# Kernel optimization log

Hardware: AMD Instinct MI355X
Metric: run time of the kernel (lower is better)

Reference implementation:

```python
import jax, jax.numpy as jnp
import numpy as np

DIM = 1024
HEADS = 16
DIM_HEAD = DIM // HEADS

def setup_inputs() -> dict:
    key = jax.random.key(0)
    k1, k2, k3 = jax.random.split(key, 3)
    x = jax.random.normal(k1, (2, 2048, DIM), dtype=jnp.float32)
    # nn.Linear(dim, 3*dim, bias=False): weight [3*dim, dim]; y = x @ W.T
    W_qkv = jax.random.normal(k2, (3 * DIM, DIM), dtype=jnp.float32) * (1.0 / np.sqrt(DIM))
    W_out = jax.random.normal(k3, (DIM, DIM), dtype=jnp.float32) * (1.0 / np.sqrt(DIM))
    return {"x": x, "W_qkv": W_qkv, "W_out": W_out}

def reference(x, W_qkv, W_out):
    b, s, _ = x.shape
    scale = DIM_HEAD ** -0.5
    qkv = x @ W_qkv.T                              # [b, s, 3*dim]
    q, k, v = jnp.split(qkv, 3, axis=-1)
    def to_heads(t):
        return t.reshape(b, s, HEADS, DIM_HEAD).transpose(0, 2, 1, 3)  # [b,h,s,d]
    q, k, v = map(to_heads, (q, k, v))
    scores = jnp.einsum('bhid,bhjd->bhij', q, k) * scale
    causal_mask = jnp.triu(jnp.ones((s, s), dtype=bool), k=1)
    scores = jnp.where(causal_mask, -jnp.inf, scores)
    attn = jax.nn.softmax(scores, axis=-1)
    out = jnp.einsum('bhij,bhjd->bhid', attn, v)
    out = out.transpose(0, 2, 1, 3).reshape(b, s, HEADS * DIM_HEAD)
    return out @ W_out.T
```

## Files before the change

kernel.cpp:

```cpp
#include <hip/hip_runtime.h>
#include <hip/hip_bf16.h>
#include <math.h>

using bf16 = __hip_bfloat16;
typedef __attribute__((ext_vector_type(8))) short bf16x8;
typedef __attribute__((ext_vector_type(4))) short bf16x4;
typedef __attribute__((ext_vector_type(4))) float f32x4;
typedef __attribute__((ext_vector_type(2))) int i32x2;

static __device__ __forceinline__ void gl_lds16(const void* g, void* l) {
  __builtin_amdgcn_global_load_lds(
      (const __attribute__((address_space(1))) unsigned int*)g,
      (__attribute__((address_space(3))) unsigned int*)l, 16, 0, 0);
}

#define MFMA16 __builtin_amdgcn_mfma_f32_16x16x32_bf16
#define MFMA16K16 __builtin_amdgcn_mfma_f32_16x16x16bf16_1k

static __device__ __forceinline__ short f2bf(float f) {
  return (short)((__builtin_bit_cast(unsigned int, f) + 0x8000u) >> 16);
}

__global__ __launch_bounds__(256) void cvt_all(
    const float* __restrict__ x, const float* __restrict__ wqkv,
    const float* __restrict__ wout, bf16* __restrict__ xb,
    bf16* __restrict__ wqkvb, bf16* __restrict__ woutb) {
  const int blk = blockIdx.x;
  const float* src;
  bf16* dst;
  int base;
  if (blk < 4096) {
    src = x; dst = xb; base = blk;
  } else if (blk < 7168) {
    src = wqkv; dst = wqkvb; base = blk - 4096;
  } else {
    src = wout; dst = woutb; base = blk - 7168;
  }
  const int i = (base * 256 + threadIdx.x) * 4;
  const float4 v = *(const float4*)(src + i);
  bf16x4 o;
  o.x = f2bf(v.x);
  o.y = f2bf(v.y);
  o.z = f2bf(v.z);
  o.w = f2bf(v.w);
  *(bf16x4*)(dst + i) = o;
}

template <int K>
static __device__ __forceinline__ void gemm_bt_acc(
    const bf16* __restrict__ A, const bf16* __restrict__ B,
    int rowA0, int rowB0, bf16* As, bf16* Bs, f32x4 acc[4][4]) {
  const int t = threadIdx.x;
  const int w = t >> 6, l = t & 63;
  const int quad = l >> 4, l16 = l & 15;
  const int wm = (w >> 1) * 64, wn = (w & 1) * 64;
  for (int k0 = 0; k0 < K; k0 += 64) {
    __syncthreads();
#pragma unroll
    for (int ii = 0; ii < 4; ii++) {
      const int c = t + ii * 256;
      const int row = c >> 3, pos = c & 7;
      const size_t off = (size_t)row * K + k0 + ((pos ^ (row & 7)) * 8);
      gl_lds16(A + (size_t)rowA0 * K + off, As + c * 8);
      gl_lds16(B + (size_t)rowB0 * K + off, Bs + c * 8);
    }
    __syncthreads();
#pragma unroll
    for (int kk2 = 0; kk2 < 2; kk2++) {
      bf16x8 af[4], bg[4];
#pragma unroll
      for (int i = 0; i < 4; i++) {
        const int rr = wm + i * 16 + l16;
        const int ci = (kk2 * 4 + quad) ^ (l16 & 7);
        af[i] = *(const bf16x8*)(As + rr * 64 + ci * 8);
      }
#pragma unroll
      for (int j = 0; j < 4; j++) {
        const int rr = wn + j * 16 + l16;
        const int ci = (kk2 * 4 + quad) ^ (l16 & 7);
        bg[j] = *(const bf16x8*)(Bs + rr * 64 + ci * 8);
      }
#pragma unroll
      for (int i = 0; i < 4; i++)
#pragma unroll
        for (int j = 0; j < 4; j++)
          acc[i][j] = MFMA16(af[i], bg[j], acc[i][j], 0, 0, 0);
    }
  }
}

__global__ __launch_bounds__(256, 3) void qkv_gemm(
    const bf16* __restrict__ x, const bf16* __restrict__ Wqkv,
    bf16* __restrict__ Qb, bf16* __restrict__ Kb, bf16* __restrict__ Vt) {
  __shared__ bf16 As[128 * 64];
  __shared__ bf16 Bs[128 * 64];
  f32x4 acc[4][4];
#pragma unroll
  for (int i = 0; i < 4; i++)
#pragma unroll
    for (int j = 0; j < 4; j++) acc[i][j] = (f32x4){0.f, 0.f, 0.f, 0.f};
  const int bm = blockIdx.x, bn = blockIdx.y;
  gemm_bt_acc<1024>(x, Wqkv, bm * 128, bn * 128, As, Bs, acc);

  const int t = threadIdx.x, w = t >> 6, l = t & 63;
  const int quad = l >> 4, l16 = l & 15;
  const int wm = (w >> 1) * 64, wn = (w & 1) * 64;
#pragma unroll
  for (int i = 0; i < 4; i++) {
    const int m0 = bm * 128 + wm + i * 16 + quad * 4;
    const int b = m0 >> 11, s0 = m0 & 2047;
#pragma unroll
    for (int j = 0; j < 4; j++) {
      const int n = bn * 128 + wn + j * 16 + l16;
      const int which = n >> 10;
      const int nn = n & 1023;
      const int h = nn >> 6, d = nn & 63;
      const int bh = b * 16 + h;
      if (which == 2) {
        bf16x4 v4;
#pragma unroll
        for (int r = 0; r < 4; r++)
          v4[r] = (short)__builtin_bit_cast(unsigned short,
                                            __float2bfloat16(acc[i][j][r]));
        *(bf16x4*)(Vt + ((size_t)bh * 64 + d) * 2048 + s0) = v4;
      } else {
        const float sc = (which == 0) ? 0.125f : 1.0f;
        bf16* dst = (which == 0) ? Qb : Kb;
#pragma unroll
        for (int r = 0; r < 4; r++)
          dst[((size_t)bh * 2048 + s0 + r) * 64 + d] =
              __float2bfloat16(acc[i][j][r] * sc);
      }
    }
  }
}

__global__ __launch_bounds__(256, 4) void attn_kernel(
    const bf16* __restrict__ Qb, const bf16* __restrict__ Kb,
    const bf16* __restrict__ Vt, bf16* __restrict__ attn) {
  __shared__ bf16 Ks[128 * 64];
  __shared__ bf16 Vts[64 * 128];
  const int x = blockIdx.x;
  const int bh = x & 31;
  const int T = x >> 5;
  const int s = T >> 3, r = T & 7;
  const int qt = s * 8 + ((s & 1) ? 7 - r : r);
  const int q0 = qt * 64;
  const int t = threadIdx.x, w = t >> 6, l = t & 63;
  const int quad = l >> 4, l16 = l & 15;
  const bf16x4 ones = {16256, 16256, 16256, 16256};
  const int b = bh >> 4, h = bh & 15;

  const int qrow = q0 + w * 16 + l16;
  const bf16* Qg = Qb + ((size_t)bh * 2048 + qrow) * 64 + quad * 8;
  bf16x8 qreg[2];
  qreg[0] = *(const bf16x8*)(Qg);
  qreg[1] = *(const bf16x8*)(Qg + 32);

  f32x4 oacc[4];
  f32x4 lacc = (f32x4){0.f, 0.f, 0.f, 0.f};
#pragma unroll
  for (int md = 0; md < 4; md++) oacc[md] = (f32x4){0.f, 0.f, 0.f, 0.f};

  const int njj = (qt + 2) >> 1;
  for (int jj = 0; jj < njj; jj++) {
    const int j0 = jj * 128;
    __syncthreads();
    const bf16* Kg = Kb + ((size_t)bh * 2048 + j0) * 64;
#pragma unroll
    for (int c = t; c < 1024; c += 256) {
      const int row = c >> 3, pos = c & 7;
      gl_lds16(Kg + (row * 8 + (pos ^ (row & 7))) * 8, Ks + c * 8);
    }
    const bf16* Vg = Vt + (size_t)bh * 64 * 2048 + j0;
#pragma unroll
    for (int c = t; c < 1024; c += 256) {
      const int d = c >> 4, pos = c & 15;
      gl_lds16(Vg + (size_t)d * 2048 + ((pos ^ (d & 15)) * 8), Vts + c * 8);
    }
    __syncthreads();

    f32x4 sacc[8];
#pragma unroll
    for (int mt = 0; mt < 8; mt++) sacc[mt] = (f32x4){0.f, 0.f, 0.f, 0.f};
#pragma unroll
    for (int kk = 0; kk < 2; kk++) {
#pragma unroll
      for (int mt = 0; mt < 8; mt++) {
        const int row = mt * 16 + l16;
        const int pos = (kk * 4 + quad) ^ (l16 & 7);
        bf16x8 kf = *(const bf16x8*)(Ks + row * 64 + pos * 8);
        sacc[mt] = MFMA16(kf, qreg[kk], sacc[mt], 0, 0, 0);
      }
    }

    bf16x4 pfrag[8];
    if (jj == njj - 1) {
#pragma unroll
      for (int mt = 0; mt < 8; mt++) {
        unsigned rb[4];
#pragma unroll
        for (int r2 = 0; r2 < 4; r2++) {
          const int sg = j0 + mt * 16 + quad * 4 + r2;
          const float p = (sg <= qrow) ? __expf(sacc[mt][r2]) : 0.f;
          rb[r2] = __builtin_bit_cast(unsigned, p) + 0x8000u;
        }
        i32x2 pk;
        pk.x = (int)__builtin_amdgcn_perm(rb[1], rb[0], 0x07060302u);
        pk.y = (int)__builtin_amdgcn_perm(rb[3], rb[2], 0x07060302u);
        pfrag[mt] = __builtin_bit_cast(bf16x4, pk);
      }
    } else {
#pragma unroll
      for (int mt = 0; mt < 8; mt++) {
        unsigned rb[4];
#pragma unroll
        for (int r2 = 0; r2 < 4; r2++) {
          const float p = __expf(sacc[mt][r2]);
          rb[r2] = __builtin_bit_cast(unsigned, p) + 0x8000u;
        }
        i32x2 pk;
        pk.x = (int)__builtin_amdgcn_perm(rb[1], rb[0], 0x07060302u);
        pk.y = (int)__builtin_amdgcn_perm(rb[3], rb[2], 0x07060302u);
        pfrag[mt] = __builtin_bit_cast(bf16x4, pk);
      }
    }

#pragma unroll
    for (int kt = 0; kt < 8; kt++) {
      lacc = MFMA16K16(ones, pfrag[kt], lacc, 0, 0, 0);
#pragma unroll
      for (int md = 0; md < 4; md++) {
        const int d = md * 16 + l16;
        const int pos = (kt * 2 + (quad >> 1)) ^ l16;
        bf16x4 va = *(const bf16x4*)(Vts + d * 128 + pos * 8 + (quad & 1) * 4);
        oacc[md] = MFMA16K16(va, pfrag[kt], oacc[md], 0, 0, 0);
      }
    }
  }

  const float inv = 1.0f / lacc[0];
#pragma unroll
  for (int md = 0; md < 4; md++) {
    bf16x4 o4;
#pragma unroll
    for (int r2 = 0; r2 < 4; r2++) o4[r2] = f2bf(oacc[md][r2] * inv);
    *(bf16x4*)(attn + ((size_t)b * 2048 + qrow) * 1024 + h * 64 + md * 16 +
               quad * 4) = o4;
  }
}

__global__ __launch_bounds__(256) void out_gemm(
    const bf16* __restrict__ attn, const bf16* __restrict__ Wout,
    float* __restrict__ out) {
  __shared__ bf16 As[128 * 32];
  __shared__ bf16 Bs[64 * 32];
  f32x4 acc[4][2];
#pragma unroll
  for (int i = 0; i < 4; i++)
#pragma unroll
    for (int j = 0; j < 2; j++) acc[i][j] = (f32x4){0.f, 0.f, 0.f, 0.f};
  const int bm = blockIdx.x, bn = blockIdx.y;
  const int t = threadIdx.x, w = t >> 6, l = t & 63;
  const int quad = l >> 4, l16 = l & 15;
  const int wm = (w >> 1) * 64, wn = (w & 1) * 32;
  const int c0 = t, c1 = t + 256;
  const bf16* a0 = attn + (size_t)(bm * 128 + (c0 >> 2)) * 1024 + (c0 & 3) * 8;
  const bf16* a1 = attn + (size_t)(bm * 128 + (c1 >> 2)) * 1024 + (c1 & 3) * 8;
  const bf16* b0 = Wout + (size_t)(bn * 64 + (t >> 2)) * 1024 + (t & 3) * 8;
  for (int k0 = 0; k0 < 1024; k0 += 32) {
    __syncthreads();
    gl_lds16(a0 + k0, As + c0 * 8);
    gl_lds16(a1 + k0, As + c1 * 8);
    gl_lds16(b0 + k0, Bs + t * 8);
    __syncthreads();
    bf16x8 af[4], bg[2];
#pragma unroll
    for (int i = 0; i < 4; i++)
      af[i] = *(const bf16x8*)(As + (wm + i * 16 + l16) * 32 + quad * 8);
#pragma unroll
    for (int j = 0; j < 2; j++)
      bg[j] = *(const bf16x8*)(Bs + (wn + j * 16 + l16) * 32 + quad * 8);
#pragma unroll
    for (int i = 0; i < 4; i++)
#pragma unroll
      for (int j = 0; j < 2; j++)
        acc[i][j] = MFMA16(af[i], bg[j], acc[i][j], 0, 0, 0);
  }
#pragma unroll
  for (int i = 0; i < 4; i++) {
#pragma unroll
    for (int j = 0; j < 2; j++) {
      const int n = bn * 64 + wn + j * 16 + l16;
#pragma unroll
      for (int r = 0; r < 4; r++) {
        const int m = bm * 128 + wm + i * 16 + quad * 4 + r;
        out[(size_t)m * 1024 + n] = acc[i][j][r];
      }
    }
  }
}

extern "C" void kernel_launch(void* const* d_in, const int* in_sizes, int n_in,
                              void* d_out, int out_size, void* d_ws, size_t ws_size,
                              hipStream_t stream) {
  const float* x = (const float*)d_in[0];
  const float* Wqkv = (const float*)d_in[1];
  const float* Wout = (const float*)d_in[2];
  float* out = (float*)d_out;

  char* ws = (char*)d_ws;
  const size_t MB = 1024 * 1024;
  bf16* xb = (bf16*)(ws + 0 * MB);
  bf16* at = (bf16*)(ws + 0 * MB);
  bf16* Wqkvb = (bf16*)(ws + 8 * MB);
  bf16* Woutb = (bf16*)(ws + 14 * MB);
  bf16* Qb = (bf16*)(ws + 16 * MB);
  bf16* Kb = (bf16*)(ws + 24 * MB);
  bf16* Vt = (bf16*)(ws + 32 * MB);

  cvt_all<<<8192, 256, 0, stream>>>(x, Wqkv, Wout, xb, Wqkvb, Woutb);
  qkv_gemm<<<dim3(32, 24), 256, 0, stream>>>(xb, Wqkvb, Qb, Kb, Vt);
  attn_kernel<<<1024, 256, 0, stream>>>(Qb, Kb, Vt, at);
  out_gemm<<<dim3(32, 16), 256, 0, stream>>>(at, Woutb, out);
}
```

Baseline: 163.8 us.

## Split KV range of long causal query tiles across two blocks with combine kernel

```diff
diff --git a/kernel.cpp b/kernel.cpp
--- a/kernel.cpp
+++ b/kernel.cpp
@@ -137,14 +137,16 @@
 
 __global__ __launch_bounds__(256, 4) void attn_kernel(
     const bf16* __restrict__ Qb, const bf16* __restrict__ Kb,
-    const bf16* __restrict__ Vt, bf16* __restrict__ attn) {
+    const bf16* __restrict__ Vt, bf16* __restrict__ attn,
+    float* __restrict__ Opart, float* __restrict__ lpart) {
   __shared__ bf16 Ks[128 * 64];
   __shared__ bf16 Vts[64 * 128];
   const int x = blockIdx.x;
   const int bh = x & 31;
-  const int T = x >> 5;
-  const int s = T >> 3, r = T & 7;
-  const int qt = s * 8 + ((s & 1) ? 7 - r : r);
+  const int u = x >> 5;
+  const bool split = u < 32;
+  const int qt = split ? 31 - (u >> 1) : 47 - u;
+  const int sp = split ? (u & 1) : 0;
   const int q0 = qt * 64;
   const int t = threadIdx.x, w = t >> 6, l = t & 63;
   const int quad = l >> 4, l16 = l & 15;
@@ -163,7 +165,13 @@
   for (int md = 0; md < 4; md++) oacc[md] = (f32x4){0.f, 0.f, 0.f, 0.f};
 
   const int njj = (qt + 2) >> 1;
-  for (int jj = 0; jj < njj; jj++) {
+  const int njj0 = njj >> 1;
+  int jlo = 0, jhi = njj;
+  if (split) {
+    if (sp) jlo = njj0;
+    else jhi = njj0;
+  }
+  for (int jj = jlo; jj < jhi; jj++) {
     const int j0 = jj * 128;
     __syncthreads();
     const bf16* Kg = Kb + ((size_t)bh * 2048 + j0) * 64;
@@ -239,14 +247,50 @@
     }
   }
 
-  const float inv = 1.0f / lacc[0];
-#pragma unroll
-  for (int md = 0; md < 4; md++) {
+  if (!split) {
+    const float inv = 1.0f / lacc[0];
+#pragma unroll
+    for (int md = 0; md < 4; md++) {
+      bf16x4 o4;
+#pragma unroll
+      for (int r2 = 0; r2 < 4; r2++) o4[r2] = f2bf(oacc[md][r2] * inv);
+      *(bf16x4*)(attn + ((size_t)b * 2048 + qrow) * 1024 + h * 64 + md * 16 +
+                 quad * 4) = o4;
+    }
+  } else {
+    float* Od =
+        Opart + (((size_t)(sp * 32 + bh) * 1024) + (qrow - 1024)) * 64;
+#pragma unroll
+    for (int md = 0; md < 4; md++)
+      *(f32x4*)(Od + md * 16 + quad * 4) = oacc[md];
+    if (quad == 0) lpart[(size_t)(sp * 32 + bh) * 1024 + (qrow - 1024)] = lacc[0];
+  }
+}
+
+__global__ __launch_bounds__(256) void attn_combine(
+    const float* __restrict__ Opart, const float* __restrict__ lpart,
+    bf16* __restrict__ attn) {
+  const int blk = blockIdx.x;
+  const int bh = blk >> 4, qi = blk & 15;
+  const int t = threadIdx.x;
+  const int r = t >> 2, dg = (t & 3) * 16;
+  const size_t rowl = (size_t)bh * 1024 + qi * 64 + r;
+  const float l0 = lpart[rowl];
+  const float l1 = lpart[(size_t)32 * 1024 + rowl];
+  const float inv = 1.0f / (l0 + l1);
+  const float* O0 = Opart + rowl * 64 + dg;
+  const float* O1 = Opart + (size_t)32 * 1024 * 64 + rowl * 64 + dg;
+  const int b = bh >> 4, h = bh & 15;
+  const int q = 1024 + qi * 64 + r;
+  bf16* dst = attn + ((size_t)b * 2048 + q) * 1024 + h * 64 + dg;
+#pragma unroll
+  for (int v = 0; v < 4; v++) {
+    const f32x4 a = *(const f32x4*)(O0 + v * 4);
+    const f32x4 c = *(const f32x4*)(O1 + v * 4);
     bf16x4 o4;
 #pragma unroll
-    for (int r2 = 0; r2 < 4; r2++) o4[r2] = f2bf(oacc[md][r2] * inv);
-    *(bf16x4*)(attn + ((size_t)b * 2048 + qrow) * 1024 + h * 64 + md * 16 +
-               quad * 4) = o4;
+    for (int e = 0; e < 4; e++) o4[e] = f2bf((a[e] + c[e]) * inv);
+    *(bf16x4*)(dst + v * 4) = o4;
   }
 }
 
@@ -318,9 +362,12 @@
   bf16* Qb = (bf16*)(ws + 16 * MB);
   bf16* Kb = (bf16*)(ws + 24 * MB);
   bf16* Vt = (bf16*)(ws + 32 * MB);
+  float* Opart = (float*)(ws + 40 * MB);
+  float* lpart = (float*)(ws + 57 * MB);
 
   cvt_all<<<8192, 256, 0, stream>>>(x, Wqkv, Wout, xb, Wqkvb, Woutb);
   qkv_gemm<<<dim3(32, 24), 256, 0, stream>>>(xb, Wqkvb, Qb, Kb, Vt);
-  attn_kernel<<<1024, 256, 0, stream>>>(Qb, Kb, Vt, at);
+  attn_kernel<<<1536, 256, 0, stream>>>(Qb, Kb, Vt, at, Opart, lpart);
+  attn_combine<<<512, 256, 0, stream>>>(Opart, lpart, at);
   out_gemm<<<dim3(32, 16), 256, 0, stream>>>(at, Woutb, out);
 }
```

Result: slower. 172.2 us (+5.1%).
